# Kernel tuning notes

Measured on AMD Instinct MI355X. Metric: run time of the kernel, lower is better.

The kernel has to match this reference:

```python
import jax, jax.numpy as jnp
import numpy as np

SIZES = [4096, 12288, 20480, 20480, 8192]  # atoms of degree 0..4 (atoms sorted by degree)
N_ATOMS = sum(SIZES)
BATCH = 1024
N_TASKS, N_CLASSES = 12, 2
BN_EPS = 1e-3  # keras BatchNormalization default epsilon


def setup_inputs() -> dict:
    key = jax.random.key(0)
    ks = jax.random.split(key, 20)
    inp = {}
    inp["atom_features"] = jax.random.normal(ks[0], (N_ATOMS, 75), jnp.float32)
    starts = np.concatenate([[0], np.cumsum(SIZES)[:-1]])
    inp["degree_slice"] = jnp.asarray(np.stack([starts, np.array(SIZES)], 1), jnp.int32)
    inp["membership"] = jax.random.randint(ks[1], (N_ATOMS,), 0, BATCH, jnp.int32)
    inp["n_samples"] = BATCH
    for d in range(1, 5):
        inp[f"deg_adj_{d}"] = jax.random.randint(ks[1 + d], (SIZES[d], d), 0, N_ATOMS, jnp.int32)

    def w(k, shape, s=0.05):
        return s * jax.random.normal(k, shape, jnp.float32)

    # GraphConv weights: order [relW_deg1, selfW_deg1, ..., relW_deg4, selfW_deg4, selfW_deg0]
    inp["gc1_W"] = w(ks[6], (9, 75, 256)); inp["gc1_b"] = w(ks[7], (9, 256))
    inp["gc2_W"] = w(ks[8], (9, 256, 256)); inp["gc2_b"] = w(ks[9], (9, 256))

    def bn_params(k, c):  # rows: gamma, beta, moving_mean, moving_var
        g = 1.0 + 0.1 * jax.random.normal(k, (c,), jnp.float32)
        b = 0.1 * jax.random.normal(jax.random.fold_in(k, 1), (c,), jnp.float32)
        return jnp.stack([g, b, jnp.zeros((c,), jnp.float32), jnp.ones((c,), jnp.float32)])

    inp["bn1"] = bn_params(ks[10], 256)
    inp["bn2"] = bn_params(ks[11], 256)
    inp["bn3"] = bn_params(ks[12], 512)
    inp["dense_W"] = w(ks[13], (256, 512)); inp["dense_b"] = w(ks[14], (512,))
    inp["head_W"] = w(ks[15], (2 * 512, N_TASKS * N_CLASSES)); inp["head_b"] = w(ks[16], (N_TASKS * N_CLASSES,))
    return inp


def _graph_conv(x, adjs, W, b):
    # degree-0 atoms: self transform only (last weight matrix)
    pieces = [x[: SIZES[0]] @ W[8] + b[8]]
    off = SIZES[0]
    for d in range(1, 5):
        nd = SIZES[d]
        self_atoms = x[off: off + nd]
        rel = jnp.take(x, adjs[d - 1], axis=0).sum(axis=1)  # [nd, F] neighbor sum
        out = rel @ W[2 * (d - 1)] + b[2 * (d - 1)] + self_atoms @ W[2 * d - 1] + b[2 * d - 1]
        pieces.append(out)
        off += nd
    return jax.nn.relu(jnp.concatenate(pieces, axis=0))


def _graph_pool(x, adjs):
    pieces = [x[: SIZES[0]]]  # degree-0: passthrough
    off = SIZES[0]
    for d in range(1, 5):
        nd = SIZES[d]
        self_atoms = x[off: off + nd]
        neigh = jnp.take(x, adjs[d - 1], axis=0)  # [nd, d, F]
        pieces.append(jnp.maximum(self_atoms, neigh.max(axis=1)))
        off += nd
    return jnp.concatenate(pieces, axis=0)


def _bn(x, p):  # inference batchnorm with moving stats
    g, b, m, v = p
    return g * (x - m) * jax.lax.rsqrt(v + BN_EPS) + b


def reference(atom_features, degree_slice, membership, n_samples,
              deg_adj_1, deg_adj_2, deg_adj_3, deg_adj_4,
              gc1_W, gc1_b, gc2_W, gc2_b, bn1, bn2, bn3,
              dense_W, dense_b, head_W, head_b):
    adjs = (deg_adj_1, deg_adj_2, deg_adj_3, deg_adj_4)
    x = atom_features
    for W, b, bn in ((gc1_W, gc1_b, bn1), (gc2_W, gc2_b, bn2)):
        x = _bn(_graph_conv(x, adjs, W, b), bn)
        x = _graph_pool(x, adjs)
    h = _bn(jax.nn.relu(x @ dense_W + dense_b), bn3)  # [N_ATOMS, 512]
    # GraphGather: per-molecule sum and max, tanh activation
    seg_sum = jax.ops.segment_sum(h, membership, num_segments=BATCH)
    seg_max = jax.ops.segment_max(h, membership, num_segments=BATCH)
    fp = jnp.tanh(jnp.concatenate([seg_sum, seg_max], axis=1))  # neural fingerprint [BATCH, 1024]
    logits = (fp @ head_W + head_b).reshape(BATCH, N_TASKS, N_CLASSES)[: int(n_samples)]  # trim
    return jax.nn.softmax(logits, axis=-1), logits, fp
```

## Files before the change

### kernel.cpp

```cpp
#include <hip/hip_runtime.h>
#include <hip/hip_bf16.h>
#include <math.h>

#define NA 65536
#define MAXSEG 160

typedef _Float16 half8 __attribute__((ext_vector_type(8)));
typedef _Float16 h4    __attribute__((ext_vector_type(4)));
typedef float float4v  __attribute__((ext_vector_type(4)));

typedef __attribute__((address_space(3))) unsigned int lds_uint;
typedef __attribute__((address_space(1))) const unsigned int g_uint;

__device__ __forceinline__ void async16(const void* g, void* l) {
    __builtin_amdgcn_global_load_lds((g_uint*)g, (lds_uint*)l, 16, 0, 0);
}


__device__ __forceinline__ int unperm128(int p) {
    return (p & ~127) + (((p & 127) & 7) << 4) + ((p & 127) >> 3);
}

__device__ __forceinline__ void atom_seg(int atom, int& d, int& loc,
                                         const int* a1, const int* a2,
                                         const int* a3, const int* a4,
                                         const int*& adj) {
    if (atom < 4096)       { d = 0; loc = 0; adj = nullptr; }
    else if (atom < 16384) { d = 1; adj = a1; loc = atom - 4096; }
    else if (atom < 36864) { d = 2; adj = a2; loc = atom - 16384; }
    else if (atom < 57344) { d = 3; adj = a3; loc = atom - 36864; }
    else                   { d = 4; adj = a4; loc = atom - 57344; }
}

__global__ void zero_count_kernel(int* __restrict__ count) {
    int i = blockIdx.x * 256 + threadIdx.x;
    if (i < 1024) count[i] = 0;
}

__global__ void bucket_kernel(const int* __restrict__ mem, int* __restrict__ count,
                              int* __restrict__ list) {
    int i = blockIdx.x * 256 + threadIdx.x;
    int seg = mem[i];
    int pos = atomicAdd(&count[seg], 1);
    if (pos < MAXSEG) list[seg * MAXSEG + pos] = i;
}

__global__ void cvt_w1_kernel(const float* __restrict__ gc1W, const float* __restrict__ gc1b,
                              _Float16* __restrict__ Wc1, float* __restrict__ bias1) {
    int idx = blockIdx.x * 256 + threadIdx.x;
    if (idx < 204800) {
        int k = idx % 160, n = (idx / 160) & 255, seg = idx / (160 * 256);
        float v = 0.f;
        if (k < 75) { int w = (seg == 0) ? 8 : (2 * seg - 1); v = gc1W[(w * 75 + k) * 256 + n]; }
        else if (k < 150 && seg > 0) { int w = 2 * (seg - 1); v = gc1W[(w * 75 + (k - 75)) * 256 + n]; }
        Wc1[(size_t)(seg * 256 + n) * 160 + k] = (_Float16)v;
    }
    if (idx < 1280) {
        int n = idx & 255, seg = idx >> 8;
        bias1[idx] = (seg == 0) ? gc1b[8 * 256 + n]
                                : gc1b[(2 * seg - 1) * 256 + n] + gc1b[2 * (seg - 1) * 256 + n];
    }
}

__global__ void cvt_w2_kernel(const float* __restrict__ gc2W, const float* __restrict__ gc2b,
                              _Float16* __restrict__ Wc2, float* __restrict__ bias2) {
    int idx = blockIdx.x * 256 + threadIdx.x;
    if (idx < 655360) {
        int k = idx & 511, n = (idx >> 9) & 255, seg = idx >> 17;
        float v = 0.f;
        if (k < 256) {
            int w = (seg == 0) ? 8 : (2 * seg - 1);
            v = gc2W[(w * 256 + unperm128(k)) * 256 + n];
        } else if (seg > 0) {
            int w = 2 * (seg - 1);
            v = gc2W[(w * 256 + unperm128(k - 256)) * 256 + n];
        }
        Wc2[(size_t)(seg * 256 + n) * 512 + k] = (_Float16)v;
    }
    if (idx < 1280) {
        int n = idx & 255, seg = idx >> 8;
        bias2[idx] = (seg == 0) ? gc2b[8 * 256 + n]
                                : gc2b[(2 * seg - 1) * 256 + n] + gc2b[2 * (seg - 1) * 256 + n];
    }
}

__global__ void cvt_wd_kernel(const float* __restrict__ dW, _Float16* __restrict__ dWt) {
    int idx = blockIdx.x * 256 + threadIdx.x;
    int n = idx >> 8, k = idx & 255;
    dWt[(size_t)n * 256 + k] = (_Float16)dW[(size_t)unperm128(k) * 512 + n];
}

__global__ void cvt_hw_kernel(const float* __restrict__ hW, float* __restrict__ hWt) {
    int idx = blockIdx.x * 256 + threadIdx.x;
    int o = idx / 1024, k = idx & 1023;
    hWt[idx] = hW[k * 24 + o];
}

__global__ __launch_bounds__(256) void gather1_kernel(
    const float* __restrict__ af,
    const int* __restrict__ a1, const int* __restrict__ a2,
    const int* __restrict__ a3, const int* __restrict__ a4,
    _Float16* __restrict__ X1) {
    int atom = blockIdx.x * 4 + (threadIdx.x >> 6);
    int lane = threadIdx.x & 63;
    int d, loc; const int* adj;
    atom_seg(atom, d, loc, a1, a2, a3, a4, adj);
    int nb[4];
    for (int j = 0; j < d; j++) nb[j] = adj[(size_t)loc * d + j];
    for (int k = lane; k < 75; k += 64) {
        X1[(size_t)atom * 160 + k] = (_Float16)af[(size_t)atom * 75 + k];
        float s = 0.f;
        for (int j = 0; j < d; j++) s += af[(size_t)nb[j] * 75 + k];
        X1[(size_t)atom * 160 + 75 + k] = (_Float16)s;
    }
    if (lane < 10) X1[(size_t)atom * 160 + 150 + lane] = (_Float16)0.f;
}

__global__ __launch_bounds__(256) void gather2n_kernel(
    const _Float16* __restrict__ p,
    const int* __restrict__ a1, const int* __restrict__ a2,
    const int* __restrict__ a3, const int* __restrict__ a4,
    _Float16* __restrict__ Xn) {
    int atom = blockIdx.x * 4 + (threadIdx.x >> 6);
    int lane = threadIdx.x & 63;
    int d, loc; const int* adj;
    atom_seg(atom, d, loc, a1, a2, a3, a4, adj);
    int nb[4];
    for (int j = 0; j < d; j++) nb[j] = adj[(size_t)loc * d + j];
    float s0 = 0.f, s1 = 0.f, s2 = 0.f, s3 = 0.f;
    for (int j = 0; j < d; j++) {
        h4 v = *(const h4*)(p + (size_t)nb[j] * 256 + lane * 4);
        s0 += (float)v[0]; s1 += (float)v[1]; s2 += (float)v[2]; s3 += (float)v[3];
    }
    h4 o; o[0] = (_Float16)s0; o[1] = (_Float16)s1; o[2] = (_Float16)s2; o[3] = (_Float16)s3;
    *(h4*)(Xn + (size_t)atom * 256 + lane * 4) = o;
}

template<int K, int N, int BK, int SPLIT>
__global__ __launch_bounds__(256) void gemm_kernel(
    const _Float16* __restrict__ X, const _Float16* __restrict__ Xn,
    const _Float16* __restrict__ Wt,
    const float* __restrict__ bias, const float* __restrict__ bnp,
    int wstride, int bstride, _Float16* __restrict__ out) {
    constexpr int NC8 = BK / 8;
    constexpr int MASK = NC8 - 1;
    __shared__ __align__(16) _Float16 As[128 * BK];
    __shared__ __align__(16) _Float16 Bs[128 * BK];
    constexpr int nb = N / 128;
    int G = gridDim.x;
    int bid = (blockIdx.x & 7) * (G >> 3) + (blockIdx.x >> 3);
    int m0 = (bid / nb) * 128, n0 = (bid % nb) * 128;
    int t = m0 >> 7;
    int seg = (t < 32) ? 0 : (t < 128) ? 1 : (t < 288) ? 2 : (t < 448) ? 3 : 4;
    const _Float16* Wb = Wt + (size_t)seg * wstride;
    const float* bia = bias + seg * bstride;
    int tid = threadIdx.x, lane = tid & 63, wave = tid >> 6;
    int wm = (wave >> 1) * 64, wn = (wave & 1) * 64;
    int lrow = lane & 15, lq = lane >> 4;
    float4v acc[4][4] = {};
    for (int kc = 0; kc < K / BK; kc++) {
        #pragma unroll
        for (int q = 0; q < NC8 / 2; q++) {
            int slot = q * 256 + wave * 64 + lane;
            int row = slot / NC8;
            int cs = slot & MASK;
            int c8 = cs ^ (row & MASK);
            const _Float16* gA;
            if (!SPLIT) {
                gA = X + (size_t)(m0 + row) * K + kc * BK + c8 * 8;
            } else {
                int kcol = kc * BK + c8 * 8;
                gA = (kcol < 256) ? X  + (size_t)(m0 + row) * 256 + kcol
                                  : Xn + (size_t)(m0 + row) * 256 + (kcol - 256);
            }
            async16(gA, As + (size_t)(q * 256 + wave * 64) * 8);
            const _Float16* gB = Wb + (size_t)(n0 + row) * K + kc * BK + c8 * 8;
            async16(gB, Bs + (size_t)(q * 256 + wave * 64) * 8);
        }
        __syncthreads();
        #pragma unroll
        for (int kl = 0; kl < BK / 32; kl++) {
            half8 af[4], bf[4];
            #pragma unroll
            for (int i = 0; i < 4; i++) {
                int ra = wm + i * 16 + lrow;
                int ca = (kl * 4 + lq) ^ (ra & MASK);
                af[i] = *(const half8*)(As + ra * BK + ca * 8);
                int rb = wn + i * 16 + lrow;
                int cb = (kl * 4 + lq) ^ (rb & MASK);
                bf[i] = *(const half8*)(Bs + rb * BK + cb * 8);
            }
            #pragma unroll
            for (int mi = 0; mi < 4; mi++)
                #pragma unroll
                for (int ni = 0; ni < 4; ni++)
                    acc[mi][ni] = __builtin_amdgcn_mfma_f32_16x16x32_f16(af[mi], bf[ni], acc[mi][ni], 0, 0, 0);
        }
        __syncthreads();
    }
    float bv[4], sc[4], mn[4], be[4];
    #pragma unroll
    for (int ni = 0; ni < 4; ni++) {
        int c = n0 + wn + ni * 16 + lrow;
        bv[ni] = bia[c];
        float g = bnp[c], vr = bnp[3 * N + c];
        mn[ni] = bnp[2 * N + c]; be[ni] = bnp[N + c];
        sc[ni] = g * rsqrtf(vr + 1e-3f);
    }
    int p0 = n0 + lrow * 8 + (wave & 1) * 4;
    #pragma unroll
    for (int mi = 0; mi < 4; mi++) {
        #pragma unroll
        for (int r = 0; r < 4; r++) {
            h4 pack;
            #pragma unroll
            for (int ni = 0; ni < 4; ni++) {
                float v = acc[mi][ni][r] + bv[ni];
                v = fmaxf(v, 0.f);
                v = sc[ni] * (v - mn[ni]) + be[ni];
                pack[ni] = (_Float16)v;
            }
            int row = m0 + wm + mi * 16 + lq * 4 + r;
            *(h4*)(out + (size_t)row * N + p0) = pack;
        }
    }
}

__global__ __launch_bounds__(256) void pool_f16_kernel(
    const _Float16* __restrict__ x,
    const int* __restrict__ a1, const int* __restrict__ a2,
    const int* __restrict__ a3, const int* __restrict__ a4,
    _Float16* __restrict__ out) {
    int atom = blockIdx.x * 4 + (threadIdx.x >> 6);
    int lane = threadIdx.x & 63;
    int d, loc; const int* adj;
    atom_seg(atom, d, loc, a1, a2, a3, a4, adj);
    h4 m = *(const h4*)(x + (size_t)atom * 256 + lane * 4);
    float m0 = (float)m[0], m1 = (float)m[1], m2 = (float)m[2], m3 = (float)m[3];
    for (int j = 0; j < d; j++) {
        int nb = adj[(size_t)loc * d + j];
        h4 v = *(const h4*)(x + (size_t)nb * 256 + lane * 4);
        m0 = fmaxf(m0, (float)v[0]); m1 = fmaxf(m1, (float)v[1]);
        m2 = fmaxf(m2, (float)v[2]); m3 = fmaxf(m3, (float)v[3]);
    }
    h4 o; o[0] = (_Float16)m0; o[1] = (_Float16)m1; o[2] = (_Float16)m2; o[3] = (_Float16)m3;
    *(h4*)(out + (size_t)atom * 256 + lane * 4) = o;
}

__global__ __launch_bounds__(512) void seg_reduce_kernel(
    const _Float16* __restrict__ h, const int* __restrict__ count,
    const int* __restrict__ list, float* __restrict__ fp) {
    int seg = blockIdx.x, c = threadIdx.x;
    int chan = unperm128(c);
    int n = count[seg]; if (n > MAXSEG) n = MAXSEG;
    float sum = 0.f, mx = -INFINITY;
    for (int a = 0; a < n; a++) {
        int row = list[seg * MAXSEG + a];
        float v = (float)h[(size_t)row * 512 + c];
        sum += v; mx = fmaxf(mx, v);
    }
    fp[(size_t)seg * 1024 + chan] = tanhf(sum);
    fp[(size_t)seg * 1024 + 512 + chan] = tanhf(mx);
}

__global__ __launch_bounds__(256) void head_kernel(
    const float* __restrict__ fp, const float* __restrict__ hWt,
    const float* __restrict__ hb, float* __restrict__ logits,
    float* __restrict__ probs) {
    __shared__ float fps[1024];
    __shared__ float red[32];
    int s = blockIdx.x;
    for (int i = threadIdx.x; i < 1024; i += 256) fps[i] = fp[(size_t)s * 1024 + i];
    __syncthreads();
    int t = threadIdx.x;
    int o = t >> 3, kp = t & 7;
    float acc = 0.f;
    if (o < 24) {
        const float* w = hWt + (size_t)o * 1024 + kp * 128;
        const float* f = fps + kp * 128;
        #pragma unroll 8
        for (int i = 0; i < 128; i++) acc = fmaf(f[i], w[i], acc);
    }
    acc += __shfl_down(acc, 4, 64);
    acc += __shfl_down(acc, 2, 64);
    acc += __shfl_down(acc, 1, 64);
    if (o < 24 && kp == 0) red[o] = acc + hb[o];
    __syncthreads();
    if (t < 24) {
        float a = red[t];
        float an = red[t ^ 1];
        logits[(size_t)s * 24 + t] = a;
        probs[(size_t)s * 24 + t] = 1.f / (1.f + expf(an - a));
    }
}

extern "C" void kernel_launch(void* const* d_in, const int* in_sizes, int n_in,
                              void* d_out, int out_size, void* d_ws, size_t ws_size,
                              hipStream_t stream) {
    const float* af         = (const float*)d_in[0];
    const int*   membership = (const int*)d_in[2];
    const int*   a1 = (const int*)d_in[4];
    const int*   a2 = (const int*)d_in[5];
    const int*   a3 = (const int*)d_in[6];
    const int*   a4 = (const int*)d_in[7];
    const float* gc1W = (const float*)d_in[8];
    const float* gc1b = (const float*)d_in[9];
    const float* gc2W = (const float*)d_in[10];
    const float* gc2b = (const float*)d_in[11];
    const float* bn1  = (const float*)d_in[12];
    const float* bn2  = (const float*)d_in[13];
    const float* bn3  = (const float*)d_in[14];
    const float* dW   = (const float*)d_in[15];
    const float* db   = (const float*)d_in[16];
    const float* hW   = (const float*)d_in[17];
    const float* hb   = (const float*)d_in[18];

    float* out    = (float*)d_out;
    float* probs  = out;
    float* logits = out + 24576;
    float* fp     = out + 49152;

    _Float16* Wc1  = (_Float16*)d_ws;
    _Float16* Wc2  = Wc1 + 204800;
    _Float16* dWt  = Wc2 + 655360;
    float* bias1   = (float*)(dWt + 131072);
    float* bias2   = bias1 + 1280;
    float* hWt     = bias2 + 1280;
    int* count     = (int*)(hWt + 24576);
    int* list      = count + 1024;
    _Float16* bufBig = (_Float16*)(list + 163840);
    _Float16* bufY   = bufBig + (size_t)NA * 512;
    _Float16* bufP   = bufY + (size_t)NA * 256;
    _Float16* X1 = bufBig;
    _Float16* Xn = bufBig + (size_t)NA * 256;
    _Float16* h  = bufBig;

    zero_count_kernel<<<4, 256, 0, stream>>>(count);
    bucket_kernel<<<256, 256, 0, stream>>>(membership, count, list);
    cvt_w1_kernel<<<800, 256, 0, stream>>>(gc1W, gc1b, Wc1, bias1);
    cvt_w2_kernel<<<2560, 256, 0, stream>>>(gc2W, gc2b, Wc2, bias2);
    cvt_wd_kernel<<<512, 256, 0, stream>>>(dW, dWt);
    cvt_hw_kernel<<<96, 256, 0, stream>>>(hW, hWt);

    gather1_kernel<<<16384, 256, 0, stream>>>(af, a1, a2, a3, a4, X1);
    gemm_kernel<160, 256, 32, 0><<<1024, 256, 0, stream>>>(X1, nullptr, Wc1, bias1, bn1,
                                                           256 * 160, 256, bufY);
    pool_f16_kernel<<<16384, 256, 0, stream>>>(bufY, a1, a2, a3, a4, bufP);
    gather2n_kernel<<<16384, 256, 0, stream>>>(bufP, a1, a2, a3, a4, Xn);
    gemm_kernel<512, 256, 64, 1><<<1024, 256, 0, stream>>>(bufP, Xn, Wc2, bias2, bn2,
                                                           256 * 512, 256, bufY);
    pool_f16_kernel<<<16384, 256, 0, stream>>>(bufY, a1, a2, a3, a4, bufP);
    gemm_kernel<256, 512, 64, 0><<<2048, 256, 0, stream>>>(bufP, nullptr, dWt, db, bn3,
                                                           0, 0, h);
    seg_reduce_kernel<<<1024, 512, 0, stream>>>(h, count, list, fp);
    head_kernel<<<1024, 256, 0, stream>>>(fp, hWt, hb, logits, probs);
}
```

Before: 348.3 us.

## Fuse prep kernels, split layer-1 gather into padded fp16 features, widen gather loads

Merges the zero-count, weight conversion and transposition kernels into one prep kernel. That kernel also converts atom features to a padded fp16 layout (80 columns). The layer-1 gather then reads this compact fp16 array with vector loads and writes only the neighbor sums. The GEMM reads self features and neighbor sums from two separate buffers through a generalized split-K parameter. The pool and gather2 kernels now use 8-wide half vectors with 32 lanes per atom. The goal is fewer launches, less traffic on scattered neighbor reads and wider memory transactions. The cost is an extra fp16 copy of the features and a re-laid-out weight matrix.

```diff
diff --git a/kernel.cpp b/kernel.cpp
--- a/kernel.cpp
+++ b/kernel.cpp
@@ -32,40 +32,46 @@
     else                   { d = 4; adj = a4; loc = atom - 57344; }
 }
 
-__global__ void zero_count_kernel(int* __restrict__ count) {
-    int i = blockIdx.x * 256 + threadIdx.x;
-    if (i < 1024) count[i] = 0;
-}
-
-__global__ void bucket_kernel(const int* __restrict__ mem, int* __restrict__ count,
-                              int* __restrict__ list) {
-    int i = blockIdx.x * 256 + threadIdx.x;
-    int seg = mem[i];
-    int pos = atomicAdd(&count[seg], 1);
-    if (pos < MAXSEG) list[seg * MAXSEG + pos] = i;
-}
-
-__global__ void cvt_w1_kernel(const float* __restrict__ gc1W, const float* __restrict__ gc1b,
-                              _Float16* __restrict__ Wc1, float* __restrict__ bias1) {
-    int idx = blockIdx.x * 256 + threadIdx.x;
-    if (idx < 204800) {
-        int k = idx % 160, n = (idx / 160) & 255, seg = idx / (160 * 256);
-        float v = 0.f;
-        if (k < 75) { int w = (seg == 0) ? 8 : (2 * seg - 1); v = gc1W[(w * 75 + k) * 256 + n]; }
-        else if (k < 150 && seg > 0) { int w = 2 * (seg - 1); v = gc1W[(w * 75 + (k - 75)) * 256 + n]; }
-        Wc1[(size_t)(seg * 256 + n) * 160 + k] = (_Float16)v;
-    }
-    if (idx < 1280) {
-        int n = idx & 255, seg = idx >> 8;
-        bias1[idx] = (seg == 0) ? gc1b[8 * 256 + n]
-                                : gc1b[(2 * seg - 1) * 256 + n] + gc1b[2 * (seg - 1) * 256 + n];
-    }
-}
-
-__global__ void cvt_w2_kernel(const float* __restrict__ gc2W, const float* __restrict__ gc2b,
-                              _Float16* __restrict__ Wc2, float* __restrict__ bias2) {
-    int idx = blockIdx.x * 256 + threadIdx.x;
-    if (idx < 655360) {
+__global__ __launch_bounds__(256) void prep_kernel(
+    const float* __restrict__ af,
+    const float* __restrict__ gc1W, const float* __restrict__ gc1b,
+    const float* __restrict__ gc2W, const float* __restrict__ gc2b,
+    const float* __restrict__ dW, const float* __restrict__ hW,
+    _Float16* __restrict__ af16, _Float16* __restrict__ Wc1, float* __restrict__ bias1,
+    _Float16* __restrict__ Wc2, float* __restrict__ bias2,
+    _Float16* __restrict__ dWt, float* __restrict__ hWt, int* __restrict__ count) {
+    int b = blockIdx.x, t = threadIdx.x;
+    if (b < 5120) {
+        int idx = b * 256 + t;
+        int atom = idx / 20, k4 = idx - atom * 20;
+        int c0 = k4 * 4;
+        h4 o;
+        #pragma unroll
+        for (int j = 0; j < 4; j++) {
+            int c = c0 + j;
+            o[j] = (_Float16)((c < 75) ? af[(size_t)atom * 75 + c] : 0.f);
+        }
+        *(h4*)(af16 + (size_t)atom * 80 + c0) = o;
+    } else if (b < 5920) {
+        int idx = (b - 5120) * 256 + t;
+        if (idx < 204800) {
+            int k = idx % 160, n = (idx / 160) & 255, seg = idx / (160 * 256);
+            float v = 0.f;
+            if (k < 80) {
+                if (k < 75) { int w = (seg == 0) ? 8 : (2 * seg - 1); v = gc1W[(w * 75 + k) * 256 + n]; }
+            } else {
+                int kk = k - 80;
+                if (kk < 75 && seg > 0) { int w = 2 * (seg - 1); v = gc1W[(w * 75 + kk) * 256 + n]; }
+            }
+            Wc1[(size_t)(seg * 256 + n) * 160 + k] = (_Float16)v;
+        }
+        if (idx < 1280) {
+            int n = idx & 255, seg = idx >> 8;
+            bias1[idx] = (seg == 0) ? gc1b[8 * 256 + n]
+                                    : gc1b[(2 * seg - 1) * 256 + n] + gc1b[2 * (seg - 1) * 256 + n];
+        }
+    } else if (b < 8480) {
+        int idx = (b - 5920) * 256 + t;
         int k = idx & 511, n = (idx >> 9) & 255, seg = idx >> 17;
         float v = 0.f;
         if (k < 256) {
@@ -76,44 +82,51 @@
             v = gc2W[(w * 256 + unperm128(k - 256)) * 256 + n];
         }
         Wc2[(size_t)(seg * 256 + n) * 512 + k] = (_Float16)v;
-    }
-    if (idx < 1280) {
-        int n = idx & 255, seg = idx >> 8;
-        bias2[idx] = (seg == 0) ? gc2b[8 * 256 + n]
-                                : gc2b[(2 * seg - 1) * 256 + n] + gc2b[2 * (seg - 1) * 256 + n];
-    }
-}
-
-__global__ void cvt_wd_kernel(const float* __restrict__ dW, _Float16* __restrict__ dWt) {
-    int idx = blockIdx.x * 256 + threadIdx.x;
-    int n = idx >> 8, k = idx & 255;
-    dWt[(size_t)n * 256 + k] = (_Float16)dW[(size_t)unperm128(k) * 512 + n];
-}
-
-__global__ void cvt_hw_kernel(const float* __restrict__ hW, float* __restrict__ hWt) {
-    int idx = blockIdx.x * 256 + threadIdx.x;
-    int o = idx / 1024, k = idx & 1023;
-    hWt[idx] = hW[k * 24 + o];
-}
-
-__global__ __launch_bounds__(256) void gather1_kernel(
-    const float* __restrict__ af,
+        if (idx < 1280) {
+            int nn = idx & 255, sg = idx >> 8;
+            bias2[idx] = (sg == 0) ? gc2b[8 * 256 + nn]
+                                   : gc2b[(2 * sg - 1) * 256 + nn] + gc2b[2 * (sg - 1) * 256 + nn];
+        }
+    } else if (b < 8992) {
+        int idx = (b - 8480) * 256 + t;
+        int n = idx >> 8, k = idx & 255;
+        dWt[(size_t)n * 256 + k] = (_Float16)dW[(size_t)unperm128(k) * 512 + n];
+    } else if (b < 9088) {
+        int idx = (b - 8992) * 256 + t;
+        int o = idx / 1024, k = idx & 1023;
+        hWt[idx] = hW[k * 24 + o];
+    } else {
+        int i = (b - 9088) * 256 + t;
+        if (i < 1024) count[i] = 0;
+    }
+}
+
+__global__ void bucket_kernel(const int* __restrict__ mem, int* __restrict__ count,
+                              int* __restrict__ list) {
+    int i = blockIdx.x * 256 + threadIdx.x;
+    int seg = mem[i];
+    int pos = atomicAdd(&count[seg], 1);
+    if (pos < MAXSEG) list[seg * MAXSEG + pos] = i;
+}
+
+__global__ __launch_bounds__(256) void gather1n_kernel(
+    const _Float16* __restrict__ af16,
     const int* __restrict__ a1, const int* __restrict__ a2,
     const int* __restrict__ a3, const int* __restrict__ a4,
-    _Float16* __restrict__ X1) {
-    int atom = blockIdx.x * 4 + (threadIdx.x >> 6);
-    int lane = threadIdx.x & 63;
+    _Float16* __restrict__ Xn1) {
+    int idx = blockIdx.x * 256 + threadIdx.x;
+    int atom = idx / 20, k4 = idx - atom * 20;
+    int c0 = k4 * 4;
     int d, loc; const int* adj;
     atom_seg(atom, d, loc, a1, a2, a3, a4, adj);
-    int nb[4];
-    for (int j = 0; j < d; j++) nb[j] = adj[(size_t)loc * d + j];
-    for (int k = lane; k < 75; k += 64) {
-        X1[(size_t)atom * 160 + k] = (_Float16)af[(size_t)atom * 75 + k];
-        float s = 0.f;
-        for (int j = 0; j < d; j++) s += af[(size_t)nb[j] * 75 + k];
-        X1[(size_t)atom * 160 + 75 + k] = (_Float16)s;
-    }
-    if (lane < 10) X1[(size_t)atom * 160 + 150 + lane] = (_Float16)0.f;
+    float s0 = 0.f, s1 = 0.f, s2 = 0.f, s3 = 0.f;
+    for (int j = 0; j < d; j++) {
+        int nb = adj[(size_t)loc * d + j];
+        h4 v = *(const h4*)(af16 + (size_t)nb * 80 + c0);
+        s0 += (float)v[0]; s1 += (float)v[1]; s2 += (float)v[2]; s3 += (float)v[3];
+    }
+    h4 o; o[0] = (_Float16)s0; o[1] = (_Float16)s1; o[2] = (_Float16)s2; o[3] = (_Float16)s3;
+    *(h4*)(Xn1 + (size_t)atom * 80 + c0) = o;
 }
 
 __global__ __launch_bounds__(256) void gather2n_kernel(
@@ -121,22 +134,24 @@
     const int* __restrict__ a1, const int* __restrict__ a2,
     const int* __restrict__ a3, const int* __restrict__ a4,
     _Float16* __restrict__ Xn) {
-    int atom = blockIdx.x * 4 + (threadIdx.x >> 6);
-    int lane = threadIdx.x & 63;
+    int atom = blockIdx.x * 8 + (threadIdx.x >> 5);
+    int l = threadIdx.x & 31;
     int d, loc; const int* adj;
     atom_seg(atom, d, loc, a1, a2, a3, a4, adj);
-    int nb[4];
-    for (int j = 0; j < d; j++) nb[j] = adj[(size_t)loc * d + j];
-    float s0 = 0.f, s1 = 0.f, s2 = 0.f, s3 = 0.f;
+    float s[8] = {};
     for (int j = 0; j < d; j++) {
-        h4 v = *(const h4*)(p + (size_t)nb[j] * 256 + lane * 4);
-        s0 += (float)v[0]; s1 += (float)v[1]; s2 += (float)v[2]; s3 += (float)v[3];
-    }
-    h4 o; o[0] = (_Float16)s0; o[1] = (_Float16)s1; o[2] = (_Float16)s2; o[3] = (_Float16)s3;
-    *(h4*)(Xn + (size_t)atom * 256 + lane * 4) = o;
-}
-
-template<int K, int N, int BK, int SPLIT>
+        int nb = adj[(size_t)loc * d + j];
+        half8 v = *(const half8*)(p + (size_t)nb * 256 + l * 8);
+        #pragma unroll
+        for (int e = 0; e < 8; e++) s[e] += (float)v[e];
+    }
+    half8 o;
+    #pragma unroll
+    for (int e = 0; e < 8; e++) o[e] = (_Float16)s[e];
+    *(half8*)(Xn + (size_t)atom * 256 + l * 8) = o;
+}
+
+template<int K, int N, int BK, int SB>
 __global__ __launch_bounds__(256) void gemm_kernel(
     const _Float16* __restrict__ X, const _Float16* __restrict__ Xn,
     const _Float16* __restrict__ Wt,
@@ -166,12 +181,12 @@
             int cs = slot & MASK;
             int c8 = cs ^ (row & MASK);
             const _Float16* gA;
-            if (!SPLIT) {
+            if (SB == 0) {
                 gA = X + (size_t)(m0 + row) * K + kc * BK + c8 * 8;
             } else {
                 int kcol = kc * BK + c8 * 8;
-                gA = (kcol < 256) ? X  + (size_t)(m0 + row) * 256 + kcol
-                                  : Xn + (size_t)(m0 + row) * 256 + (kcol - 256);
+                gA = (kcol < SB) ? X  + (size_t)(m0 + row) * SB + kcol
+                                 : Xn + (size_t)(m0 + row) * SB + (kcol - SB);
             }
             async16(gA, As + (size_t)(q * 256 + wave * 64) * 8);
             const _Float16* gB = Wb + (size_t)(n0 + row) * K + kc * BK + c8 * 8;
@@ -231,20 +246,24 @@
     const int* __restrict__ a1, const int* __restrict__ a2,
     const int* __restrict__ a3, const int* __restrict__ a4,
     _Float16* __restrict__ out) {
-    int atom = blockIdx.x * 4 + (threadIdx.x >> 6);
-    int lane = threadIdx.x & 63;
+    int atom = blockIdx.x * 8 + (threadIdx.x >> 5);
+    int l = threadIdx.x & 31;
     int d, loc; const int* adj;
     atom_seg(atom, d, loc, a1, a2, a3, a4, adj);
-    h4 m = *(const h4*)(x + (size_t)atom * 256 + lane * 4);
-    float m0 = (float)m[0], m1 = (float)m[1], m2 = (float)m[2], m3 = (float)m[3];
+    half8 m = *(const half8*)(x + (size_t)atom * 256 + l * 8);
+    float mv[8];
+    #pragma unroll
+    for (int e = 0; e < 8; e++) mv[e] = (float)m[e];
     for (int j = 0; j < d; j++) {
         int nb = adj[(size_t)loc * d + j];
-        h4 v = *(const h4*)(x + (size_t)nb * 256 + lane * 4);
-        m0 = fmaxf(m0, (float)v[0]); m1 = fmaxf(m1, (float)v[1]);
-        m2 = fmaxf(m2, (float)v[2]); m3 = fmaxf(m3, (float)v[3]);
-    }
-    h4 o; o[0] = (_Float16)m0; o[1] = (_Float16)m1; o[2] = (_Float16)m2; o[3] = (_Float16)m3;
-    *(h4*)(out + (size_t)atom * 256 + lane * 4) = o;
+        half8 v = *(const half8*)(x + (size_t)nb * 256 + l * 8);
+        #pragma unroll
+        for (int e = 0; e < 8; e++) mv[e] = fmaxf(mv[e], (float)v[e]);
+    }
+    half8 o;
+    #pragma unroll
+    for (int e = 0; e < 8; e++) o[e] = (_Float16)mv[e];
+    *(half8*)(out + (size_t)atom * 256 + l * 8) = o;
 }
 
 __global__ __launch_bounds__(512) void seg_reduce_kernel(
@@ -331,25 +350,22 @@
     _Float16* bufBig = (_Float16*)(list + 163840);
     _Float16* bufY   = bufBig + (size_t)NA * 512;
     _Float16* bufP   = bufY + (size_t)NA * 256;
-    _Float16* X1 = bufBig;
-    _Float16* Xn = bufBig + (size_t)NA * 256;
-    _Float16* h  = bufBig;
-
-    zero_count_kernel<<<4, 256, 0, stream>>>(count);
+    _Float16* af16 = bufBig;
+    _Float16* Xn1  = bufBig + (size_t)NA * 80;
+    _Float16* Xn   = bufBig + (size_t)NA * 256;
+    _Float16* h    = bufBig;
+
+    prep_kernel<<<9092, 256, 0, stream>>>(af, gc1W, gc1b, gc2W, gc2b, dW, hW,
+                                          af16, Wc1, bias1, Wc2, bias2, dWt, hWt, count);
     bucket_kernel<<<256, 256, 0, stream>>>(membership, count, list);
-    cvt_w1_kernel<<<800, 256, 0, stream>>>(gc1W, gc1b, Wc1, bias1);
-    cvt_w2_kernel<<<2560, 256, 0, stream>>>(gc2W, gc2b, Wc2, bias2);
-    cvt_wd_kernel<<<512, 256, 0, stream>>>(dW, dWt);
-    cvt_hw_kernel<<<96, 256, 0, stream>>>(hW, hWt);
-
-    gather1_kernel<<<16384, 256, 0, stream>>>(af, a1, a2, a3, a4, X1);
-    gemm_kernel<160, 256, 32, 0><<<1024, 256, 0, stream>>>(X1, nullptr, Wc1, bias1, bn1,
-                                                           256 * 160, 256, bufY);
-    pool_f16_kernel<<<16384, 256, 0, stream>>>(bufY, a1, a2, a3, a4, bufP);
-    gather2n_kernel<<<16384, 256, 0, stream>>>(bufP, a1, a2, a3, a4, Xn);
-    gemm_kernel<512, 256, 64, 1><<<1024, 256, 0, stream>>>(bufP, Xn, Wc2, bias2, bn2,
-                                                           256 * 512, 256, bufY);
-    pool_f16_kernel<<<16384, 256, 0, stream>>>(bufY, a1, a2, a3, a4, bufP);
+    gather1n_kernel<<<5120, 256, 0, stream>>>(af16, a1, a2, a3, a4, Xn1);
+    gemm_kernel<160, 256, 32, 80><<<1024, 256, 0, stream>>>(af16, Xn1, Wc1, bias1, bn1,
+                                                            256 * 160, 256, bufY);
+    pool_f16_kernel<<<8192, 256, 0, stream>>>(bufY, a1, a2, a3, a4, bufP);
+    gather2n_kernel<<<8192, 256, 0, stream>>>(bufP, a1, a2, a3, a4, Xn);
+    gemm_kernel<512, 256, 64, 256><<<1024, 256, 0, stream>>>(bufP, Xn, Wc2, bias2, bn2,
+                                                             256 * 512, 256, bufY);
+    pool_f16_kernel<<<8192, 256, 0, stream>>>(bufY, a1, a2, a3, a4, bufP);
     gemm_kernel<256, 512, 64, 0><<<2048, 256, 0, stream>>>(bufP, nullptr, dWt, db, bn3,
                                                            0, 0, h);
     seg_reduce_kernel<<<1024, 512, 0, stream>>>(h, count, list, fp);
```

After: 311.8 us. 10.5% less time.
